# Optimization experiments

Measured on AMD Instinct MI355X. Metric: run time of the kernel, lower is better.

Reference implementation:

```python
import jax, jax.numpy as jnp
import numpy as np

NUM_REL = 6
EMBED_DIM = 128
B, N = 8, 1024


def _relation_type(dx, dy):
    # Faithful to _get_relation_type's if/elif chain (order matters).
    return jnp.select(
        [dy > 0.5,
         dy < -0.5,
         dx < -0.5,
         dx > 0.5,
         (jnp.abs(dx) < 0.3) & (jnp.abs(dy) < 0.3)],
        [0, 1, 2, 3, 4],
        5,
    )


def setup_inputs() -> dict:
    key = jax.random.key(0)
    k1, k2, k3, k4 = jax.random.split(key, 4)
    symbols = jax.random.normal(k1, (B, N, EMBED_DIM), dtype=jnp.float32)
    positions = jax.random.normal(k2, (B, N, 2), dtype=jnp.float32)
    # 6 Linear(embed_dim, embed_dim) layers, stacked: W [6, D, D] (torch layout: y = x @ W.T + b)
    bound = 1.0 / np.sqrt(EMBED_DIM)
    W = jax.random.uniform(k3, (NUM_REL, EMBED_DIM, EMBED_DIM), dtype=jnp.float32,
                           minval=-bound, maxval=bound)
    b = jax.random.uniform(k4, (NUM_REL, EMBED_DIM), dtype=jnp.float32,
                           minval=-bound, maxval=bound)
    return {"symbols": symbols, "positions": positions, "W": W, "b": b}


def reference(symbols, positions, W, b):
    Bn, Nn, D = symbols.shape
    # dx[b,i,j] = pos[b,j,0] - pos[b,i,0]; dy likewise (source i -> target j)
    dx = positions[:, None, :, 0] - positions[:, :, None, 0]  # [B, i, j]
    dy = positions[:, None, :, 1] - positions[:, :, None, 1]
    rel = _relation_type(dx, dy)  # [B, i, j] in {0..5}

    # Per-type transform of every source symbol: T[r,b,i,:] = symbols[b,i] @ W[r].T + b[r]
    T = jnp.einsum('bid,red->rbie', symbols, W) + b[:, None, None, :]  # [6, B, N, D]

    # One-hot relation mask with i != j excluded; scatter-add into targets j.
    not_diag = ~jnp.eye(Nn, dtype=bool)  # [i, j]
    mask = (rel[None] == jnp.arange(NUM_REL)[:, None, None, None]) & not_diag  # [6, B, i, j]
    agg = jnp.einsum('rbij,rbie->bje', mask.astype(symbols.dtype), T)  # [B, N, D]
    return symbols + agg
```

## Files before the change

### kernel.cpp

```cpp
#include <hip/hip_runtime.h>
#include <stdint.h>


typedef __attribute__((ext_vector_type(8))) short bf16x8;
typedef __attribute__((ext_vector_type(4))) float f32x4;
union U4B { uint4 u; bf16x8 b; };

#if defined(__has_builtin)
#  if __has_builtin(__builtin_amdgcn_global_load_lds)
#    define HAVE_GLL 1
#  endif
#  if __has_builtin(__builtin_amdgcn_mul_u24)
#    define OH_MUL24 1
#  endif
#endif

__device__ __forceinline__ uint16_t f2bf(float f) {
    union { float f; uint32_t u; } v; v.f = f;
    uint32_t u = v.u;
    uint32_t r = (u + 0x7FFFu + ((u >> 16) & 1u)) >> 16;
    return (uint16_t)r;
}

__global__ __launch_bounds__(256)
void prep_kernel(const float* __restrict__ X, const float* __restrict__ W,
                 uint16_t* __restrict__ symT, uint16_t* __restrict__ WtB) {
    const int blk = blockIdx.x, tid = threadIdx.x;
    if (blk < 256) {
        __shared__ float T[64 * 65];
        const int b = blk & 7, z = blk >> 3, it = z & 15, et = z >> 4;
        const int i0 = it * 64, e0 = et * 64;
        const float4* Xf = (const float4*)X;
#pragma unroll
        for (int s = 0; s < 4; ++s) {
            int il = s * 16 + (tid >> 4), e4 = tid & 15;
            float4 v = Xf[((size_t)b << 15) + (size_t)((i0 + il) << 5) + (e0 >> 2) + e4];
            T[il * 65 + e4 * 4 + 0] = v.x;
            T[il * 65 + e4 * 4 + 1] = v.y;
            T[il * 65 + e4 * 4 + 2] = v.z;
            T[il * 65 + e4 * 4 + 3] = v.w;
        }
        __syncthreads();
#pragma unroll
        for (int s = 0; s < 4; ++s) {
            int el = s * 16 + (tid >> 4), il4 = tid & 15;
            uint16_t h0 = f2bf(T[(il4 * 4 + 0) * 65 + el]);
            uint16_t h1 = f2bf(T[(il4 * 4 + 1) * 65 + el]);
            uint16_t h2 = f2bf(T[(il4 * 4 + 2) * 65 + el]);
            uint16_t h3 = f2bf(T[(il4 * 4 + 3) * 65 + el]);
            uint2 pk = { (uint32_t)h0 | ((uint32_t)h1 << 16),
                         (uint32_t)h2 | ((uint32_t)h3 << 16) };
            *(uint2*)&symT[((size_t)b << 17) + ((size_t)(e0 + el) << 10) + i0 + il4 * 4] = pk;
        }
    } else {
        int g = (blk - 256) * 256 + tid;
        float4 v = ((const float4*)W)[g];
        int r = g >> 12, rem = g & 4095, ep = rem >> 5, e4 = rem & 31;
        int kb = r * 4 + (e4 >> 3);
        int kc = (e4 & 7) * 4;
        uint16_t h0 = f2bf(v.x), h1 = f2bf(v.y), h2 = f2bf(v.z), h3 = f2bf(v.w);
        uint2 pk = { (uint32_t)h0 | ((uint32_t)h1 << 16),
                     (uint32_t)h2 | ((uint32_t)h3 << 16) };
        *(uint2*)&WtB[((size_t)(kb * 128 + ep)) * 32 + kc] = pk;
    }
}

#define SP 776

__global__ __launch_bounds__(512)
void fused_kernel(const float* __restrict__ sym, const float* __restrict__ pos,
                  const uint16_t* __restrict__ symT, const uint16_t* __restrict__ WtB,
                  const float* __restrict__ bias, float* __restrict__ out) {
    __shared__ __align__(16) char smem[81920];
    uint16_t* symTS   = (uint16_t*)smem;
    float2*   posS    = (float2*)(smem + 32768);
    uint16_t* SA      = (uint16_t*)smem;
    float*    partial = (float*)(smem + 24832);
    uint32_t* rel32   = (uint32_t*)(smem + 65536);

    const int blk = blockIdx.x;
    const int b = blk & 7, jt = blk >> 3, j0 = jt * 16;
    const int tid = threadIdx.x;
    const int w = tid >> 6, lane = tid & 63, m = lane & 15, q = lane >> 4;

    const uint16_t* symTb = symT + ((size_t)b << 17);

    int goff[4];
#pragma unroll
    for (int s = 0; s < 4; ++s) {
        int c16 = s * 512 + tid;
        int e = c16 >> 4, sg = (c16 & 15) ^ (e & 15);
        goff[s] = (e << 10) + sg * 8;
    }
    const int lwb = w * 1024;

    auto issue_chunk = [&](int cidx, int bufsel) {
#ifdef HAVE_GLL
#pragma unroll
        for (int s = 0; s < 4; ++s) {
            const uint16_t* gp = symTb + goff[s] + cidx * 128;
            char* lp = smem + bufsel * 32768 + s * 8192 + lwb;
            typedef const __attribute__((address_space(1))) uint32_t gu32;
            typedef __attribute__((address_space(3))) uint32_t lu32;
            __builtin_amdgcn_global_load_lds((gu32*)gp, (lu32*)lp, 16, 0, 0);
        }
#else
#pragma unroll
        for (int s = 0; s < 4; ++s) {
            uint4 v = *(const uint4*)(symTb + goff[s] + cidx * 128);
            *(uint4*)(smem + bufsel * 32768 + (s * 512 + tid) * 16) = v;
        }
#endif
    };

    issue_chunk(0, 0);

    const float2* pos2 = (const float2*)pos + ((size_t)b << 10);
    posS[tid] = pos2[tid];
    posS[tid + 512] = pos2[tid + 512];
    __syncthreads();

    {
        const int mm = tid & 15, grp = tid >> 4;
        const int j = j0 + mm;
        const float2 pj = posS[j];
        uint32_t* dst = &rel32[mm * 256];
        const int sw = mm * 2;
#pragma unroll
        for (int s = 0; s < 8; ++s) {
            uint32_t word = 0;
#pragma unroll
            for (int qq = 0; qq < 4; ++qq) {
                int i = grp * 32 + s * 4 + qq;
                float2 pi = posS[i];
                float dx = pj.x - pi.x, dy = pj.y - pi.y;
                int r = (dy > 0.5f) ? 0
                      : (dy < -0.5f) ? 1
                      : (dx < -0.5f) ? 2
                      : (dx > 0.5f)  ? 3
                      : (fabsf(dx) < 0.3f && fabsf(dy) < 0.3f) ? 4
                      : 5;
                uint32_t oh = (i == j) ? 0u : (1u << r);
                word |= oh << (8 * qq);
            }
            dst[(grp * 8 + s) ^ sw] = word;
        }
    }
    __syncthreads();

    f32x4 acc[6];
#pragma unroll
    for (int r = 0; r < 6; ++r) acc[r] = (f32x4){0.f, 0.f, 0.f, 0.f};

    const int E = w * 16 + m;
    const int esw = E & 15;
    const int csw = m * 2;

    for (int c = 0; c < 8; ++c) {
        if (c < 7) issue_chunk(c + 1, (c + 1) & 1);
        const uint16_t* bt = symTS + ((c & 1) << 14) + E * 128;
        const uint32_t* crow = &rel32[m * 256 + c * 32];
#pragma unroll
        for (int ks = 0; ks < 4; ++ks) {
            U4B bfr;
            bfr.u = *(const uint4*)(bt + ((((ks << 2) + q) ^ esw) << 3));
            uint2 cw = *(const uint2*)&crow[(((ks << 3) + (q << 1)) ^ csw)];
            uint32_t hx01 = __builtin_amdgcn_perm(cw.x, cw.x, 0x01010000u) & 0x00FF00FFu;
            uint32_t hx23 = __builtin_amdgcn_perm(cw.x, cw.x, 0x03030202u) & 0x00FF00FFu;
            uint32_t hy01 = __builtin_amdgcn_perm(cw.y, cw.y, 0x01010000u) & 0x00FF00FFu;
            uint32_t hy23 = __builtin_amdgcn_perm(cw.y, cw.y, 0x03030202u) & 0x00FF00FFu;
#pragma unroll
            for (int r = 0; r < 6; ++r) {
                const uint32_t rm = 0x00010001u << r;
                U4B a;
#ifdef OH_MUL24
                const uint32_t mc = 0x3F80u >> r;
                a.u.x = (uint32_t)__builtin_amdgcn_mul_u24((int)(hx01 & rm), (int)mc);
                a.u.y = (uint32_t)__builtin_amdgcn_mul_u24((int)(hx23 & rm), (int)mc);
                a.u.z = (uint32_t)__builtin_amdgcn_mul_u24((int)(hy01 & rm), (int)mc);
                a.u.w = (uint32_t)__builtin_amdgcn_mul_u24((int)(hy23 & rm), (int)mc);
#else
                uint32_t g2;
                g2 = hx01 & rm; a.u.x = (g2 << (14 - r)) - (g2 << (7 - r));
                g2 = hx23 & rm; a.u.y = (g2 << (14 - r)) - (g2 << (7 - r));
                g2 = hy01 & rm; a.u.z = (g2 << (14 - r)) - (g2 << (7 - r));
                g2 = hy23 & rm; a.u.w = (g2 << (14 - r)) - (g2 << (7 - r));
#endif
                acc[r] = __builtin_amdgcn_mfma_f32_16x16x32_bf16(a.b, bfr.b, acc[r], 0, 0, 0);
            }
        }
        __syncthreads();
    }

#pragma unroll
    for (int r = 0; r < 6; ++r)
#pragma unroll
        for (int reg = 0; reg < 4; ++reg)
            SA[(q * 4 + reg) * SP + r * 128 + w * 16 + m] = f2bf(acc[r][reg]);
    __syncthreads();

    {
        const int g = w >> 1, h = w & 1;
        f32x4 c2[4];
#pragma unroll
        for (int nf = 0; nf < 4; ++nf) c2[nf] = (f32x4){0.f, 0.f, 0.f, 0.f};
#pragma unroll
        for (int kf = 0; kf < 6; ++kf) {
            U4B af;
            af.u = *(const uint4*)&SA[m * SP + g * 192 + kf * 32 + q * 8];
            const int kb = g * 6 + kf;
#pragma unroll
            for (int nf = 0; nf < 4; ++nf) {
                U4B bw;
                bw.u = *(const uint4*)&WtB[((size_t)(kb * 128 + h * 64 + nf * 16 + m)) * 32 + q * 8];
                c2[nf] = __builtin_amdgcn_mfma_f32_16x16x32_bf16(af.b, bw.b, c2[nf], 0, 0, 0);
            }
        }
#pragma unroll
        for (int nf = 0; nf < 4; ++nf)
#pragma unroll
            for (int reg = 0; reg < 4; ++reg)
                partial[g * 2112 + (q * 4 + reg) * 132 + h * 64 + nf * 16 + m] = c2[nf][reg];
    }
    __syncthreads();

    {
        const int j = tid >> 5, t = tid & 31, e0 = t << 2;
        const uint32_t* row = &rel32[j * 256 + t * 8];
        uint32_t s0 = 0, s1 = 0, s2 = 0, s3 = 0, s4 = 0, s5 = 0;
#pragma unroll
        for (int k = 0; k < 8; ++k) {
            uint32_t wd = row[k];
            s0 += wd & 0x01010101u;        s1 += (wd >> 1) & 0x01010101u;
            s2 += (wd >> 2) & 0x01010101u; s3 += (wd >> 3) & 0x01010101u;
            s4 += (wd >> 4) & 0x01010101u; s5 += (wd >> 5) & 0x01010101u;
        }
        int cnt[6];
        cnt[0] = (int)((s0 * 0x01010101u) >> 24);
        cnt[1] = (int)((s1 * 0x01010101u) >> 24);
        cnt[2] = (int)((s2 * 0x01010101u) >> 24);
        cnt[3] = (int)((s3 * 0x01010101u) >> 24);
        cnt[4] = (int)((s4 * 0x01010101u) >> 24);
        cnt[5] = (int)((s5 * 0x01010101u) >> 24);
#pragma unroll
        for (int off = 1; off < 32; off <<= 1)
#pragma unroll
            for (int r = 0; r < 6; ++r)
                cnt[r] += __shfl_xor(cnt[r], off, 64);

        float4 a4 = {0.f, 0.f, 0.f, 0.f};
#pragma unroll
        for (int g4 = 0; g4 < 4; ++g4) {
            float4 u = *(const float4*)&partial[g4 * 2112 + j * 132 + e0];
            a4.x += u.x; a4.y += u.y; a4.z += u.z; a4.w += u.w;
        }
#pragma unroll
        for (int r = 0; r < 6; ++r) {
            float cf = (float)cnt[r];
            float4 bb = *(const float4*)&bias[r * 128 + e0];
            a4.x += cf * bb.x; a4.y += cf * bb.y; a4.z += cf * bb.z; a4.w += cf * bb.w;
        }
        size_t o = ((size_t)(b * 1024 + j0 + j) << 7) + e0;
        float4 sv = *(const float4*)&sym[o];
        float4 ov = { sv.x + a4.x, sv.y + a4.y, sv.z + a4.z, sv.w + a4.w };
        *(float4*)&out[o] = ov;
    }
}

extern "C" void kernel_launch(void* const* d_in, const int* in_sizes, int n_in,
                              void* d_out, int out_size, void* d_ws, size_t ws_size,
                              hipStream_t stream) {
    const float* symbols   = (const float*)d_in[0];
    const float* positions = (const float*)d_in[1];
    const float* W         = (const float*)d_in[2];
    const float* bias      = (const float*)d_in[3];
    float* out             = (float*)d_out;

    char* ws = (char*)d_ws;
    uint16_t* symT = (uint16_t*)ws;
    uint16_t* WtB  = (uint16_t*)(ws + 2097152);

    prep_kernel<<<352, 256, 0, stream>>>(symbols, W, symT, WtB);
    fused_kernel<<<512, 512, 0, stream>>>(symbols, positions, symT, WtB, bias, out);
}
```

Baseline: 93.20 us.

## Derive sixth relation aggregate from column sums and relax barriers

Adds a per-batch column-sum pass to the prep kernel. The fused kernel now computes only five relation aggregates with MFMA and recovers the sixth as the total minus the diagonal term minus the other five, cutting the one-hot MFMA work by a sixth. It also reorganises the LDS staging so each wave loads its own rows, replaces the per-chunk __syncthreads with vmcnt waits plus lgkm-only barriers, and sets an occupancy hint on launch bounds. The subtraction for the sixth relation adds fp32 cancellation error before bf16 rounding, and the relaxed synchronisation depends on each wave consuming only the LDS data it loaded itself.

```diff
diff --git a/kernel.cpp b/kernel.cpp
--- a/kernel.cpp
+++ b/kernel.cpp
@@ -22,9 +22,16 @@
     return (uint16_t)r;
 }
 
+#define BARRIER_LGKM() do {                                   \
+    asm volatile("s_waitcnt lgkmcnt(0)" ::: "memory");        \
+    __builtin_amdgcn_s_barrier();                             \
+    asm volatile("" ::: "memory");                            \
+} while (0)
+
 __global__ __launch_bounds__(256)
 void prep_kernel(const float* __restrict__ X, const float* __restrict__ W,
-                 uint16_t* __restrict__ symT, uint16_t* __restrict__ WtB) {
+                 uint16_t* __restrict__ symT, uint16_t* __restrict__ WtB,
+                 float* __restrict__ T4) {
     const int blk = blockIdx.x, tid = threadIdx.x;
     if (blk < 256) {
         __shared__ float T[64 * 65];
@@ -52,7 +59,7 @@
                          (uint32_t)h2 | ((uint32_t)h3 << 16) };
             *(uint2*)&symT[((size_t)b << 17) + ((size_t)(e0 + el) << 10) + i0 + il4 * 4] = pk;
         }
-    } else {
+    } else if (blk < 352) {
         int g = (blk - 256) * 256 + tid;
         float4 v = ((const float4*)W)[g];
         int r = g >> 12, rem = g & 4095, ep = rem >> 5, e4 = rem & 31;
@@ -62,15 +69,27 @@
         uint2 pk = { (uint32_t)h0 | ((uint32_t)h1 << 16),
                      (uint32_t)h2 | ((uint32_t)h3 << 16) };
         *(uint2*)&WtB[((size_t)(kb * 128 + ep)) * 32 + kc] = pk;
+    } else {
+        const int z = blk - 352, bb = z >> 2, qq = z & 3;
+        const int e = tid & 127, half = tid >> 7;
+        const float* base = X + (((size_t)(bb << 10) + (qq << 8) + (half << 7)) << 7) + e;
+        float s = 0.f;
+#pragma unroll 8
+        for (int itr = 0; itr < 128; ++itr) s += base[(size_t)itr << 7];
+        __shared__ float red[256];
+        red[tid] = s;
+        __syncthreads();
+        if (tid < 128) T4[(z << 7) + tid] = red[tid] + red[tid + 128];
     }
 }
 
 #define SP 776
 
-__global__ __launch_bounds__(512)
+__global__ __launch_bounds__(512, 4)
 void fused_kernel(const float* __restrict__ sym, const float* __restrict__ pos,
                   const uint16_t* __restrict__ symT, const uint16_t* __restrict__ WtB,
-                  const float* __restrict__ bias, float* __restrict__ out) {
+                  const float* __restrict__ bias, const float* __restrict__ T4,
+                  float* __restrict__ out) {
     __shared__ __align__(16) char smem[81920];
     uint16_t* symTS   = (uint16_t*)smem;
     float2*   posS    = (float2*)(smem + 32768);
@@ -88,18 +107,18 @@
     int goff[4];
 #pragma unroll
     for (int s = 0; s < 4; ++s) {
-        int c16 = s * 512 + tid;
-        int e = c16 >> 4, sg = (c16 & 15) ^ (e & 15);
-        goff[s] = (e << 10) + sg * 8;
-    }
-    const int lwb = w * 1024;
+        int e = (w << 4) + (s << 2) + (lane >> 4);
+        int sg = (lane & 15) ^ (e & 15);
+        goff[s] = (e << 10) + (sg << 3);
+    }
+    const int lwb = w << 12;
 
     auto issue_chunk = [&](int cidx, int bufsel) {
 #ifdef HAVE_GLL
 #pragma unroll
         for (int s = 0; s < 4; ++s) {
             const uint16_t* gp = symTb + goff[s] + cidx * 128;
-            char* lp = smem + bufsel * 32768 + s * 8192 + lwb;
+            char* lp = smem + bufsel * 32768 + lwb + s * 1024;
             typedef const __attribute__((address_space(1))) uint32_t gu32;
             typedef __attribute__((address_space(3))) uint32_t lu32;
             __builtin_amdgcn_global_load_lds((gu32*)gp, (lu32*)lp, 16, 0, 0);
@@ -108,17 +127,17 @@
 #pragma unroll
         for (int s = 0; s < 4; ++s) {
             uint4 v = *(const uint4*)(symTb + goff[s] + cidx * 128);
-            *(uint4*)(smem + bufsel * 32768 + (s * 512 + tid) * 16) = v;
+            *(uint4*)(smem + bufsel * 32768 + lwb + s * 1024 + lane * 16) = v;
         }
 #endif
     };
 
+    const float2* pos2 = (const float2*)pos + ((size_t)b << 10);
+    float2 p0 = pos2[tid], p1 = pos2[tid + 512];
     issue_chunk(0, 0);
-
-    const float2* pos2 = (const float2*)pos + ((size_t)b << 10);
-    posS[tid] = pos2[tid];
-    posS[tid + 512] = pos2[tid + 512];
-    __syncthreads();
+    posS[tid] = p0;
+    posS[tid + 512] = p1;
+    BARRIER_LGKM();
 
     {
         const int mm = tid & 15, grp = tid >> 4;
@@ -146,18 +165,23 @@
             dst[(grp * 8 + s) ^ sw] = word;
         }
     }
-    __syncthreads();
-
-    f32x4 acc[6];
-#pragma unroll
-    for (int r = 0; r < 6; ++r) acc[r] = (f32x4){0.f, 0.f, 0.f, 0.f};
-
-    const int E = w * 16 + m;
-    const int esw = E & 15;
+    BARRIER_LGKM();
+
+    f32x4 acc[5];
+#pragma unroll
+    for (int r = 0; r < 5; ++r) acc[r] = (f32x4){0.f, 0.f, 0.f, 0.f};
+
+    const int E = (w << 4) + m;
+    const int esw = m;
     const int csw = m * 2;
 
     for (int c = 0; c < 8; ++c) {
-        if (c < 7) issue_chunk(c + 1, (c + 1) & 1);
+        if (c < 7) {
+            issue_chunk(c + 1, (c + 1) & 1);
+            asm volatile("s_waitcnt vmcnt(4)" ::: "memory");
+        } else {
+            asm volatile("s_waitcnt vmcnt(0)" ::: "memory");
+        }
         const uint16_t* bt = symTS + ((c & 1) << 14) + E * 128;
         const uint32_t* crow = &rel32[m * 256 + c * 32];
 #pragma unroll
@@ -170,7 +194,7 @@
             uint32_t hy01 = __builtin_amdgcn_perm(cw.y, cw.y, 0x01010000u) & 0x00FF00FFu;
             uint32_t hy23 = __builtin_amdgcn_perm(cw.y, cw.y, 0x03030202u) & 0x00FF00FFu;
 #pragma unroll
-            for (int r = 0; r < 6; ++r) {
+            for (int r = 0; r < 5; ++r) {
                 const uint32_t rm = 0x00010001u << r;
                 U4B a;
 #ifdef OH_MUL24
@@ -189,15 +213,26 @@
                 acc[r] = __builtin_amdgcn_mfma_f32_16x16x32_bf16(a.b, bfr.b, acc[r], 0, 0, 0);
             }
         }
-        __syncthreads();
-    }
-
-#pragma unroll
-    for (int r = 0; r < 6; ++r)
+    }
+    BARRIER_LGKM();
+
+#pragma unroll
+    for (int r = 0; r < 5; ++r)
 #pragma unroll
         for (int reg = 0; reg < 4; ++reg)
-            SA[(q * 4 + reg) * SP + r * 128 + w * 16 + m] = f2bf(acc[r][reg]);
-    __syncthreads();
+            SA[(q * 4 + reg) * SP + r * 128 + E] = f2bf(acc[r][reg]);
+    {
+        float ts = T4[((b << 2) + 0) * 128 + E] + T4[((b << 2) + 1) * 128 + E]
+                 + T4[((b << 2) + 2) * 128 + E] + T4[((b << 2) + 3) * 128 + E];
+#pragma unroll
+        for (int reg = 0; reg < 4; ++reg) {
+            float symj = sym[((size_t)((b << 10) + j0 + (q << 2) + reg) << 7) + E];
+            float s5 = ts - symj
+                     - acc[0][reg] - acc[1][reg] - acc[2][reg] - acc[3][reg] - acc[4][reg];
+            SA[(q * 4 + reg) * SP + 5 * 128 + E] = f2bf(s5);
+        }
+    }
+    BARRIER_LGKM();
 
     {
         const int g = w >> 1, h = w & 1;
@@ -222,18 +257,18 @@
             for (int reg = 0; reg < 4; ++reg)
                 partial[g * 2112 + (q * 4 + reg) * 132 + h * 64 + nf * 16 + m] = c2[nf][reg];
     }
-    __syncthreads();
+    BARRIER_LGKM();
 
     {
         const int j = tid >> 5, t = tid & 31, e0 = t << 2;
         const uint32_t* row = &rel32[j * 256 + t * 8];
-        uint32_t s0 = 0, s1 = 0, s2 = 0, s3 = 0, s4 = 0, s5 = 0;
+        uint32_t s0 = 0, s1 = 0, s2 = 0, s3 = 0, s4 = 0;
 #pragma unroll
         for (int k = 0; k < 8; ++k) {
             uint32_t wd = row[k];
             s0 += wd & 0x01010101u;        s1 += (wd >> 1) & 0x01010101u;
             s2 += (wd >> 2) & 0x01010101u; s3 += (wd >> 3) & 0x01010101u;
-            s4 += (wd >> 4) & 0x01010101u; s5 += (wd >> 5) & 0x01010101u;
+            s4 += (wd >> 4) & 0x01010101u;
         }
         int cnt[6];
         cnt[0] = (int)((s0 * 0x01010101u) >> 24);
@@ -241,12 +276,12 @@
         cnt[2] = (int)((s2 * 0x01010101u) >> 24);
         cnt[3] = (int)((s3 * 0x01010101u) >> 24);
         cnt[4] = (int)((s4 * 0x01010101u) >> 24);
-        cnt[5] = (int)((s5 * 0x01010101u) >> 24);
 #pragma unroll
         for (int off = 1; off < 32; off <<= 1)
 #pragma unroll
-            for (int r = 0; r < 6; ++r)
+            for (int r = 0; r < 5; ++r)
                 cnt[r] += __shfl_xor(cnt[r], off, 64);
+        cnt[5] = 1023 - cnt[0] - cnt[1] - cnt[2] - cnt[3] - cnt[4];
 
         float4 a4 = {0.f, 0.f, 0.f, 0.f};
 #pragma unroll
@@ -279,7 +314,8 @@
     char* ws = (char*)d_ws;
     uint16_t* symT = (uint16_t*)ws;
     uint16_t* WtB  = (uint16_t*)(ws + 2097152);
-
-    prep_kernel<<<352, 256, 0, stream>>>(symbols, W, symT, WtB);
-    fused_kernel<<<512, 512, 0, stream>>>(symbols, positions, symT, WtB, bias, out);
+    float*    T4   = (float*)(ws + 2097152 + 196608);
+
+    prep_kernel<<<384, 256, 0, stream>>>(symbols, W, symT, WtB, T4);
+    fused_kernel<<<512, 512, 0, stream>>>(symbols, positions, symT, WtB, bias, T4, out);
 }
```

Measured after the change: 94.00 us. Within noise of the previous version (+0.9%).
